# Performance work log

Measured on AMD Instinct MI355X. Metric: run time of the kernel, lower is better.

The kernel has to match this reference:

```python
import jax, jax.numpy as jnp
import numpy as np
import math

NUM_CLASSES = 80
IOU_LOSS_THRESH = 0.5
ANCHORS = [
    np.array([[12, 16], [19, 36], [40, 28]], dtype=np.float32),
    np.array([[36, 75], [76, 55], [72, 146]], dtype=np.float32),
    np.array([[142, 110], [192, 243], [459, 401]], dtype=np.float32),
]


def decode(conv, anchors, stride, num_class):
    B, S = conv.shape[0], conv.shape[1]
    A = anchors.shape[0]
    conv = conv.reshape(B, S, S, A, 5 + num_class)
    dxdy = conv[..., 0:2]
    dwdh = conv[..., 2:4]
    dconf = conv[..., 4:5]
    dprob = conv[..., 5:]
    r = jnp.arange(S, dtype=conv.dtype)
    # matches torch: offset[..., 0] varies along dim2, offset[..., 1] along dim1
    offset = jnp.stack([jnp.broadcast_to(r[None, :], (S, S)),
                        jnp.broadcast_to(r[:, None], (S, S))], axis=-1)
    offset = offset[None, :, :, None, :]  # (1,S,S,1,2)
    pred_xy = (jax.nn.sigmoid(dxdy) + offset) * stride
    pred_wh = jnp.exp(dwdh) * jnp.asarray(anchors)  # (A,2) broadcast
    return jnp.concatenate([pred_xy, pred_wh,
                            jax.nn.sigmoid(dconf), jax.nn.sigmoid(dprob)], axis=-1)


def _to_corners(b):
    return jnp.concatenate([b[..., :2] - b[..., 2:] * 0.5,
                            b[..., :2] + b[..., 2:] * 0.5], axis=-1)


def bbox_ciou(boxes1, boxes2):
    b1 = _to_corners(boxes1)
    b2 = _to_corners(boxes2)
    b1 = jnp.concatenate([jnp.minimum(b1[..., :2], b1[..., 2:]),
                          jnp.maximum(b1[..., :2], b1[..., 2:])], axis=-1)
    b2 = jnp.concatenate([jnp.minimum(b2[..., :2], b2[..., 2:]),
                          jnp.maximum(b2[..., :2], b2[..., 2:])], axis=-1)
    area1 = (b1[..., 2] - b1[..., 0]) * (b1[..., 3] - b1[..., 1])
    area2 = (b2[..., 2] - b2[..., 0]) * (b2[..., 3] - b2[..., 1])
    lu = jnp.maximum(b1[..., :2], b2[..., :2])
    rd = jnp.minimum(b1[..., 2:], b2[..., 2:])
    inter = jnp.maximum(rd - lu, 0.0)
    inter_area = inter[..., 0] * inter[..., 1]
    union = area1 + area2 - inter_area
    iou = inter_area / (union + 1e-9)
    enc_lu = jnp.minimum(b1[..., :2], b2[..., :2])
    enc_rd = jnp.maximum(b1[..., 2:], b2[..., 2:])
    enc_wh = enc_rd - enc_lu
    c2 = enc_wh[..., 0] ** 2 + enc_wh[..., 1] ** 2
    p2 = (boxes1[..., 0] - boxes2[..., 0]) ** 2 + (boxes1[..., 1] - boxes2[..., 1]) ** 2
    atan1 = jnp.arctan(boxes1[..., 2] / (boxes1[..., 3] + 1e-9))
    atan2 = jnp.arctan(boxes2[..., 2] / (boxes2[..., 3] + 1e-9))
    v = 4.0 * (atan1 - atan2) ** 2 / (math.pi ** 2)
    a = v / (1.0 - iou + v)
    return iou - p2 / c2 - a * v


def bbox_iou(boxes1, boxes2):
    area1 = boxes1[..., 2] * boxes1[..., 3]
    area2 = boxes2[..., 2] * boxes2[..., 3]
    b1 = _to_corners(boxes1)
    b2 = _to_corners(boxes2)
    lu = jnp.maximum(b1[..., :2], b2[..., :2])
    rd = jnp.minimum(b1[..., 2:], b2[..., 2:])
    inter = jnp.maximum(rd - lu, 0.0)
    inter_area = inter[..., 0] * inter[..., 1]
    union = area1 + area2 - inter_area
    return inter_area / union


def loss_layer(conv, pred, label, bboxes, stride, num_class, iou_loss_thresh):
    B, S = conv.shape[0], conv.shape[1]
    input_size = float(stride * S)
    pred_xywh = pred[..., 0:4]
    pred_conf = pred[..., 4:5]
    pred_prob = pred[..., 5:]
    label_xywh = label[..., 0:4]
    respond_bbox = label[..., 4:5]
    label_prob = label[..., 5:]

    ciou = bbox_ciou(pred_xywh, label_xywh)[..., None]  # (B,S,S,3,1)
    bbox_loss_scale = 2.0 - label_xywh[..., 2:3] * label_xywh[..., 3:4] / input_size ** 2
    ciou_loss = respond_bbox * bbox_loss_scale * (1.0 - ciou)

    prob_pos = label_prob * (-jnp.log(pred_prob + 1e-9))
    prob_neg = (1.0 - label_prob) * (-jnp.log(1.0 - pred_prob + 1e-9))
    prob_loss = respond_bbox * (prob_pos + prob_neg)

    iou = bbox_iou(pred_xywh[:, :, :, :, None, :],
                   bboxes[:, None, None, None, :, :])  # (B,S,S,3,70)
    max_iou = jnp.max(iou, axis=-1, keepdims=True)
    respond_bgd = (1.0 - respond_bbox) * (max_iou < iou_loss_thresh).astype(pred.dtype)
    pos_loss = respond_bbox * (-jnp.log(pred_conf + 1e-9))
    neg_loss = respond_bgd * (-jnp.log(1.0 - pred_conf + 1e-9))
    conf_loss = pos_loss + neg_loss

    ciou_loss = ciou_loss.sum(axis=(1, 2, 3, 4)).mean()
    conf_loss = conf_loss.sum(axis=(1, 2, 3, 4)).mean()
    prob_loss = prob_loss.sum(axis=(1, 2, 3, 4)).mean()
    return ciou_loss, conf_loss, prob_loss


def setup_inputs() -> dict:
    key = jax.random.key(0)
    ks = jax.random.split(key, 7)
    B, NC = 16, NUM_CLASSES
    C = 3 * (5 + NC)
    inp = {
        'conv_lbbox': jax.random.normal(ks[0], (B, 19, 19, C), jnp.float32),
        'conv_mbbox': jax.random.normal(ks[1], (B, 38, 38, C), jnp.float32),
        'conv_sbbox': jax.random.normal(ks[2], (B, 76, 76, C), jnp.float32),
        'label_sbbox': jax.random.uniform(ks[3], (B, 76, 76, 3, 5 + NC), jnp.float32),
        'label_mbbox': jax.random.uniform(ks[4], (B, 38, 38, 3, 5 + NC), jnp.float32),
        'label_lbbox': jax.random.uniform(ks[5], (B, 19, 19, 3, 5 + NC), jnp.float32),
        'true_bboxes': jax.random.uniform(ks[6], (B, 70, 4), jnp.float32, 1.0, 600.0),
    }
    return inp


def reference(conv_lbbox, conv_mbbox, conv_sbbox, label_sbbox, label_mbbox,
              label_lbbox, true_bboxes):
    nc, thr = NUM_CLASSES, IOU_LOSS_THRESH
    pred_s = decode(conv_sbbox, ANCHORS[0], 8, nc)
    pred_m = decode(conv_mbbox, ANCHORS[1], 16, nc)
    pred_l = decode(conv_lbbox, ANCHORS[2], 32, nc)
    s_ciou, s_conf, s_prob = loss_layer(conv_sbbox, pred_s, label_sbbox, true_bboxes, 8, nc, thr)
    m_ciou, m_conf, m_prob = loss_layer(conv_mbbox, pred_m, label_mbbox, true_bboxes, 16, nc, thr)
    l_ciou, l_conf, l_prob = loss_layer(conv_lbbox, pred_l, label_lbbox, true_bboxes, 32, nc, thr)
    ciou_loss = s_ciou + m_ciou + l_ciou
    conf_loss = s_conf + m_conf + l_conf
    prob_loss = s_prob + m_prob + l_prob
    all_loss = ciou_loss + conf_loss + prob_loss
    return (all_loss, ciou_loss, conf_loss, prob_loss)
```

## Files before the change

### kernel.cpp

```cpp
#include <hip/hip_runtime.h>
#include <math.h>

#define NCLS 80
#define CH 85

static constexpr int RS = 16 * 76 * 76 * 3;
static constexpr int RM = 16 * 38 * 38 * 3;
static constexpr int RL = 16 * 19 * 19 * 3;

static constexpr int RECB = 128;
static constexpr int BS_BLK = RS / RECB;
static constexpr int BM_BLK = (RM + RECB - 1) / RECB;
static constexpr int BL_BLK = (RL + RECB - 1) / RECB;
static constexpr int NBLK   = BS_BLK + BM_BLK + BL_BLK;

static constexpr int N4_FULL = RECB * CH / 4;
static constexpr int K_FULL  = N4_FULL / 256;
static constexpr int TAIL_T  = N4_FULL - K_FULL * 256;

__constant__ float c_anchors[18] = {
    12.f, 16.f, 19.f, 36.f, 40.f, 28.f,
    36.f, 75.f, 76.f, 55.f, 72.f, 146.f,
    142.f, 110.f, 192.f, 243.f, 459.f, 401.f
};

__device__ __forceinline__ float fast_rcp(float x) {
    return __builtin_amdgcn_rcpf(x);
}
__device__ __forceinline__ float sigm(float x) {
    return fast_rcp(1.f + __expf(-x));
}
__device__ __forceinline__ float softplusf(float x) {
    return fmaxf(x, 0.f) + __logf(1.f + __expf(-fabsf(x)));
}

__global__ __launch_bounds__(256, 6) void yolo_main(
    const float* __restrict__ conv_l, const float* __restrict__ conv_m,
    const float* __restrict__ conv_s, const float* __restrict__ lab_s,
    const float* __restrict__ lab_m, const float* __restrict__ lab_l,
    const float* __restrict__ tb, float* __restrict__ pb)
{
    int blk = blockIdx.x;

    const float* conv; const float* lab;
    int S; float stride; int ao; int blkLocal; int nrec_scale;
    if (blk < BS_BLK) {
        conv = conv_s; lab = lab_s; S = 76; stride = 8.f;  ao = 0;
        blkLocal = blk;                 nrec_scale = RS;
    } else if (blk < BS_BLK + BM_BLK) {
        conv = conv_m; lab = lab_m; S = 38; stride = 16.f; ao = 6;
        blkLocal = blk - BS_BLK;        nrec_scale = RM;
    } else {
        conv = conv_l; lab = lab_l; S = 19; stride = 32.f; ao = 12;
        blkLocal = blk - BS_BLK - BM_BLK; nrec_scale = RL;
    }

    int r0   = blkLocal * RECB;
    int nrec = min(RECB, nrec_scale - r0);
    int n4   = (nrec * CH) >> 2;

    const float* cbase = conv + (size_t)r0 * CH;
    const float* lbase = lab  + (size_t)r0 * CH;

    __shared__ float resp_s[RECB + 4];
    __shared__ float red[4][3];

    int t = threadIdx.x;

    float resp = 0.f;
    float c0 = 0.f, c1 = 0.f, c2v = 0.f, c3 = 0.f, c4 = 0.f;
    float l0 = 0.f, l1 = 0.f, l2 = 0.f, l3 = 0.f;
    if (t < nrec) {
        const float* cr = cbase + (size_t)t * CH;
        const float* lr = lbase + (size_t)t * CH;
        resp = lr[4];
        c0 = cr[0]; c1 = cr[1]; c2v = cr[2]; c3 = cr[3]; c4 = cr[4];
        l0 = lr[0]; l1 = lr[1]; l2 = lr[2]; l3 = lr[3];
    }
    if (t <= RECB) resp_s[t] = (t < nrec) ? resp : 0.f;
    __syncthreads();

    float prob_acc = 0.f;

    auto do4 = [&](int i4) {
        int e = i4 << 2;
        float4 cv = *reinterpret_cast<const float4*>(cbase + e);
        float4 lv = *reinterpret_cast<const float4*>(lbase + e);
        unsigned rA  = (unsigned)e / 85u;
        unsigned rem = (rA + 1u) * 85u - (unsigned)e;
        float respA = resp_s[rA];
        float respB = resp_s[rA + 1u];
        float r1v = (rem <= 1u) ? respB : respA;
        float r2v = (rem <= 2u) ? respB : respA;
        float r3v = (rem <= 3u) ? respB : respA;
        prob_acc = fmaf(respA, fmaf(-lv.x, cv.x, softplusf(cv.x)), prob_acc);
        prob_acc = fmaf(r1v,   fmaf(-lv.y, cv.y, softplusf(cv.y)), prob_acc);
        prob_acc = fmaf(r2v,   fmaf(-lv.z, cv.z, softplusf(cv.z)), prob_acc);
        prob_acc = fmaf(r3v,   fmaf(-lv.w, cv.w, softplusf(cv.w)), prob_acc);
    };

    if (n4 == N4_FULL) {
        #pragma unroll 5
        for (int k = 0; k < K_FULL; ++k) do4(t + 256 * k);
        if (t < TAIL_T) do4(t + 256 * K_FULL);
    } else {
        for (int i4 = t; i4 < n4; i4 += 256) do4(i4);
    }

    float ciou_acc = 0.f, conf_acc = 0.f;
    if (t < nrec) {
        float corr = fmaf(-l0,   c0,  softplusf(c0))
                   + fmaf(-l1,   c1,  softplusf(c1))
                   + fmaf(-l2,   c2v, softplusf(c2v))
                   + fmaf(-l3,   c3,  softplusf(c3))
                   + fmaf(-resp, c4,  softplusf(c4));
        prob_acc = fmaf(-resp, corr, prob_acc);

        unsigned rl = (unsigned)(r0 + t);
        unsigned a = rl % 3u; unsigned q = rl / 3u;
        unsigned j = q % (unsigned)S; q /= (unsigned)S;
        unsigned i = q % (unsigned)S; unsigned b = q / (unsigned)S;

        float lx = l0, ly = l1, lw = l2, lh = l3;

        float px = (sigm(c0) + (float)j) * stride;
        float py = (sigm(c1) + (float)i) * stride;
        float pw = __expf(c2v) * c_anchors[ao + 2 * a];
        float ph = __expf(c3)  * c_anchors[ao + 2 * a + 1];

        float hx = 0.5f * pw, hy = 0.5f * ph;
        float b1x1 = px - hx, b1y1 = py - hy, b1x2 = px + hx, b1y2 = py + hy;
        float hlx = 0.5f * lw, hly = 0.5f * lh;
        float b2x1 = lx - hlx, b2y1 = ly - hly, b2x2 = lx + hlx, b2y2 = ly + hly;

        float area1 = (b1x2 - b1x1) * (b1y2 - b1y1);
        float area2 = (b2x2 - b2x1) * (b2y2 - b2y1);
        float lux = fmaxf(b1x1, b2x1), luy = fmaxf(b1y1, b2y1);
        float rdx = fminf(b1x2, b2x2), rdy = fminf(b1y2, b2y2);
        float iw = fmaxf(rdx - lux, 0.f), ih = fmaxf(rdy - luy, 0.f);
        float inter = iw * ih;
        float uni = area1 + area2 - inter;
        float iou = inter / (uni + 1e-9f);

        float encw = fmaxf(b1x2, b2x2) - fminf(b1x1, b2x1);
        float ench = fmaxf(b1y2, b2y2) - fminf(b1y1, b2y1);
        float cc2 = encw * encw + ench * ench;
        float dx = px - lx, dy = py - ly;
        float p2 = dx * dx + dy * dy;
        float at1 = atanf(pw / (ph + 1e-9f));
        float at2 = atanf(lw / (lh + 1e-9f));
        float dat = at1 - at2;
        const float FOUR_OVER_PI2 = 0.40528473456935109f;
        float v = FOUR_OVER_PI2 * dat * dat;
        float al = v / (1.f - iou + v);
        float ciou = iou - p2 / cc2 - al * v;
        float bscale = 2.f - lw * lh * (1.f / (608.f * 608.f));
        ciou_acc = resp * bscale * (1.f - ciou);

        const float4* tb4 = reinterpret_cast<const float4*>(tb) + (size_t)b * 70;
        float parea = pw * ph;
        float maxiou = 0.f;
        #pragma unroll 5
        for (int n = 0; n < 70; n++) {
            float4 tbx = tb4[n];
            float tx = tbx.x, ty = tbx.y, tw = tbx.z, th = tbx.w;
            float tx1 = tx - 0.5f * tw, ty1 = ty - 0.5f * th;
            float tx2 = tx + 0.5f * tw, ty2 = ty + 0.5f * th;
            float ix1 = fmaxf(b1x1, tx1), iy1 = fmaxf(b1y1, ty1);
            float ix2 = fminf(b1x2, tx2), iy2 = fminf(b1y2, ty2);
            float iiw = fmaxf(ix2 - ix1, 0.f), iih = fmaxf(iy2 - iy1, 0.f);
            float ia = iiw * iih;
            float u = parea + tw * th - ia;
            maxiou = fmaxf(maxiou, ia * fast_rcp(u));
        }
        float rbgd = (1.f - resp) * (maxiou < 0.5f ? 1.f : 0.f);
        float spc = softplusf(c4);
        conf_acc = resp * (spc - c4) + rbgd * spc;
    }

    for (int off = 32; off > 0; off >>= 1) {
        ciou_acc += __shfl_down(ciou_acc, off);
        conf_acc += __shfl_down(conf_acc, off);
        prob_acc += __shfl_down(prob_acc, off);
    }
    int lane = threadIdx.x & 63, wv = threadIdx.x >> 6;
    if (lane == 0) { red[wv][0] = ciou_acc; red[wv][1] = conf_acc; red[wv][2] = prob_acc; }
    __syncthreads();
    if (threadIdx.x == 0) {
        pb[blk]            = red[0][0] + red[1][0] + red[2][0] + red[3][0];
        pb[NBLK + blk]     = red[0][1] + red[1][1] + red[2][1] + red[3][1];
        pb[2 * NBLK + blk] = red[0][2] + red[1][2] + red[2][2] + red[3][2];
    }
}

__global__ __launch_bounds__(256) void finalize_k(const float* __restrict__ pb,
                                                  float* __restrict__ out)
{
    double s0 = 0.0, s1 = 0.0, s2 = 0.0;
    for (int i = threadIdx.x; i < NBLK; i += 256) {
        s0 += (double)pb[i];
        s1 += (double)pb[NBLK + i];
        s2 += (double)pb[2 * NBLK + i];
    }
    for (int off = 32; off > 0; off >>= 1) {
        s0 += __shfl_down(s0, off);
        s1 += __shfl_down(s1, off);
        s2 += __shfl_down(s2, off);
    }
    __shared__ double rd[4][3];
    int lane = threadIdx.x & 63, wv = threadIdx.x >> 6;
    if (lane == 0) { rd[wv][0] = s0; rd[wv][1] = s1; rd[wv][2] = s2; }
    __syncthreads();
    if (threadIdx.x == 0) {
        float ci = (float)((rd[0][0] + rd[1][0] + rd[2][0] + rd[3][0]) / 16.0);
        float co = (float)((rd[0][1] + rd[1][1] + rd[2][1] + rd[3][1]) / 16.0);
        float pr = (float)((rd[0][2] + rd[1][2] + rd[2][2] + rd[3][2]) / 16.0);
        out[0] = ci + co + pr;
        out[1] = ci;
        out[2] = co;
        out[3] = pr;
    }
}

extern "C" void kernel_launch(void* const* d_in, const int* in_sizes, int n_in,
                              void* d_out, int out_size, void* d_ws, size_t ws_size,
                              hipStream_t stream) {
    const float* conv_l = (const float*)d_in[0];
    const float* conv_m = (const float*)d_in[1];
    const float* conv_s = (const float*)d_in[2];
    const float* lab_s  = (const float*)d_in[3];
    const float* lab_m  = (const float*)d_in[4];
    const float* lab_l  = (const float*)d_in[5];
    const float* tb     = (const float*)d_in[6];
    float* pb  = (float*)d_ws;
    float* out = (float*)d_out;

    yolo_main<<<NBLK, 256, 0, stream>>>(conv_l, conv_m, conv_s,
                                        lab_s, lab_m, lab_l, tb, pb);
    finalize_k<<<1, 256, 0, stream>>>(pb, out);
}
```

Baseline: 273.8 us.

## Software-pipeline prob loss loads and drop shared-memory resp staging barrier

After: 278.1 us. Within noise of the previous version (+1.6%).

```diff
diff --git a/kernel.cpp b/kernel.cpp
--- a/kernel.cpp
+++ b/kernel.cpp
@@ -1,7 +1,6 @@
 #include <hip/hip_runtime.h>
 #include <math.h>
 
-#define NCLS 80
 #define CH 85
 
 static constexpr int RS = 16 * 76 * 76 * 3;
@@ -15,7 +14,7 @@
 static constexpr int NBLK   = BS_BLK + BM_BLK + BL_BLK;
 
 static constexpr int N4_FULL = RECB * CH / 4;
-static constexpr int K_FULL  = N4_FULL / 256;
+static constexpr int K_FULL  = 10;
 static constexpr int TAIL_T  = N4_FULL - K_FULL * 256;
 
 __constant__ float c_anchors[18] = {
@@ -34,7 +33,54 @@
     return fmaxf(x, 0.f) + __logf(1.f + __expf(-fabsf(x)));
 }
 
-__global__ __launch_bounds__(256, 6) void yolo_main(
+
+template<int CNT>
+__device__ __forceinline__ void load_stage(const float* __restrict__ cbase,
+                                           const float* __restrict__ lbase,
+                                           int nrec, const int (&i4s)[CNT],
+                                           const bool (&act)[CNT],
+                                           float4 (&cv)[CNT], float4 (&lv)[CNT],
+                                           float (&ra)[CNT], float (&rb)[CNT])
+{
+    #pragma unroll
+    for (int u = 0; u < CNT; ++u) {
+        int e = i4s[u] << 2;
+        cv[u] = *reinterpret_cast<const float4*>(cbase + e);
+        lv[u] = *reinterpret_cast<const float4*>(lbase + e);
+        unsigned rA  = (unsigned)e / 85u;
+        unsigned rBi = rA + 1u;
+        unsigned rmx = (unsigned)(nrec - 1);
+        rBi = (rBi > rmx) ? rmx : rBi;
+        float a = lbase[rA * 85u + 4u];
+        float b = lbase[rBi * 85u + 4u];
+        ra[u] = act[u] ? a : 0.f;
+        rb[u] = act[u] ? b : 0.f;
+    }
+}
+
+template<int CNT>
+__device__ __forceinline__ void comp_stage(const int (&i4s)[CNT],
+                                           const float4 (&cv)[CNT], const float4 (&lv)[CNT],
+                                           const float (&ra)[CNT], const float (&rb)[CNT],
+                                           float& prob_acc)
+{
+    #pragma unroll
+    for (int u = 0; u < CNT; ++u) {
+        int e = i4s[u] << 2;
+        unsigned rA  = (unsigned)e / 85u;
+        unsigned rem = (rA + 1u) * 85u - (unsigned)e;
+        float respA = ra[u], respB = rb[u];
+        float r1 = (rem <= 1u) ? respB : respA;
+        float r2 = (rem <= 2u) ? respB : respA;
+        float r3 = (rem <= 3u) ? respB : respA;
+        prob_acc = fmaf(respA, fmaf(-lv[u].x, cv[u].x, softplusf(cv[u].x)), prob_acc);
+        prob_acc = fmaf(r1,    fmaf(-lv[u].y, cv[u].y, softplusf(cv[u].y)), prob_acc);
+        prob_acc = fmaf(r2,    fmaf(-lv[u].z, cv[u].z, softplusf(cv[u].z)), prob_acc);
+        prob_acc = fmaf(r3,    fmaf(-lv[u].w, cv[u].w, softplusf(cv[u].w)), prob_acc);
+    }
+}
+
+__global__ __launch_bounds__(256, 4) void yolo_main(
     const float* __restrict__ conv_l, const float* __restrict__ conv_m,
     const float* __restrict__ conv_s, const float* __restrict__ lab_s,
     const float* __restrict__ lab_m, const float* __restrict__ lab_l,
@@ -62,52 +108,64 @@
     const float* cbase = conv + (size_t)r0 * CH;
     const float* lbase = lab  + (size_t)r0 * CH;
 
-    __shared__ float resp_s[RECB + 4];
-    __shared__ float red[4][3];
-
     int t = threadIdx.x;
 
-    float resp = 0.f;
+    float prob_acc = 0.f, ciou_acc = 0.f, conf_acc = 0.f;
     float c0 = 0.f, c1 = 0.f, c2v = 0.f, c3 = 0.f, c4 = 0.f;
-    float l0 = 0.f, l1 = 0.f, l2 = 0.f, l3 = 0.f;
-    if (t < nrec) {
-        const float* cr = cbase + (size_t)t * CH;
-        const float* lr = lbase + (size_t)t * CH;
-        resp = lr[4];
-        c0 = cr[0]; c1 = cr[1]; c2v = cr[2]; c3 = cr[3]; c4 = cr[4];
-        l0 = lr[0]; l1 = lr[1]; l2 = lr[2]; l3 = lr[3];
-    }
-    if (t <= RECB) resp_s[t] = (t < nrec) ? resp : 0.f;
-    __syncthreads();
-
-    float prob_acc = 0.f;
-
-    auto do4 = [&](int i4) {
-        int e = i4 << 2;
-        float4 cv = *reinterpret_cast<const float4*>(cbase + e);
-        float4 lv = *reinterpret_cast<const float4*>(lbase + e);
-        unsigned rA  = (unsigned)e / 85u;
-        unsigned rem = (rA + 1u) * 85u - (unsigned)e;
-        float respA = resp_s[rA];
-        float respB = resp_s[rA + 1u];
-        float r1v = (rem <= 1u) ? respB : respA;
-        float r2v = (rem <= 2u) ? respB : respA;
-        float r3v = (rem <= 3u) ? respB : respA;
-        prob_acc = fmaf(respA, fmaf(-lv.x, cv.x, softplusf(cv.x)), prob_acc);
-        prob_acc = fmaf(r1v,   fmaf(-lv.y, cv.y, softplusf(cv.y)), prob_acc);
-        prob_acc = fmaf(r2v,   fmaf(-lv.z, cv.z, softplusf(cv.z)), prob_acc);
-        prob_acc = fmaf(r3v,   fmaf(-lv.w, cv.w, softplusf(cv.w)), prob_acc);
-    };
+    float l0 = 0.f, l1 = 0.f, l2 = 0.f, l3 = 0.f, resp = 0.f;
 
     if (n4 == N4_FULL) {
-        #pragma unroll 5
-        for (int k = 0; k < K_FULL; ++k) do4(t + 256 * k);
-        if (t < TAIL_T) do4(t + 256 * K_FULL);
+        int  iA[4] = { t,          t + 256,    t + 512,    t + 768  };
+        int  iB[4] = { t + 1024,   t + 1280,   t + 1536,   t + 1792 };
+        bool tl    = (t < TAIL_T);
+        int  iC[3] = { t + 2048,   t + 2304,   tl ? (t + 2560) : t };
+        bool a4[4] = { true, true, true, true };
+        bool aC[3] = { true, true, tl };
+
+        float4 cvA[4], lvA[4]; float raA[4], rbA[4];
+        float4 cvB[4], lvB[4]; float raB[4], rbB[4];
+        float4 cvC[3], lvC[3]; float raC[3], rbC[3];
+
+        load_stage<4>(cbase, lbase, nrec, iA, a4, cvA, lvA, raA, rbA);
+        load_stage<4>(cbase, lbase, nrec, iB, a4, cvB, lvB, raB, rbB);
+        comp_stage<4>(iA, cvA, lvA, raA, rbA, prob_acc);
+        load_stage<3>(cbase, lbase, nrec, iC, aC, cvC, lvC, raC, rbC);
+        comp_stage<4>(iB, cvB, lvB, raB, rbB, prob_acc);
+        if (t < RECB) {
+            const float* cr = cbase + t * CH;
+            const float* lr = lbase + t * CH;
+            c0 = cr[0]; c1 = cr[1]; c2v = cr[2]; c3 = cr[3]; c4 = cr[4];
+            l0 = lr[0]; l1 = lr[1]; l2  = lr[2]; l3 = lr[3]; resp = lr[4];
+        }
+        comp_stage<3>(iC, cvC, lvC, raC, rbC, prob_acc);
     } else {
-        for (int i4 = t; i4 < n4; i4 += 256) do4(i4);
-    }
-
-    float ciou_acc = 0.f, conf_acc = 0.f;
+        for (int i4 = t; i4 < n4; i4 += 256) {
+            int e = i4 << 2;
+            float4 cv = *reinterpret_cast<const float4*>(cbase + e);
+            float4 lv = *reinterpret_cast<const float4*>(lbase + e);
+            unsigned rA  = (unsigned)e / 85u;
+            unsigned rem = (rA + 1u) * 85u - (unsigned)e;
+            unsigned rBi = rA + 1u;
+            unsigned rmx = (unsigned)(nrec - 1);
+            rBi = (rBi > rmx) ? rmx : rBi;
+            float respA = lbase[rA * 85u + 4u];
+            float respB = lbase[rBi * 85u + 4u];
+            float r1 = (rem <= 1u) ? respB : respA;
+            float r2 = (rem <= 2u) ? respB : respA;
+            float r3 = (rem <= 3u) ? respB : respA;
+            prob_acc = fmaf(respA, fmaf(-lv.x, cv.x, softplusf(cv.x)), prob_acc);
+            prob_acc = fmaf(r1,    fmaf(-lv.y, cv.y, softplusf(cv.y)), prob_acc);
+            prob_acc = fmaf(r2,    fmaf(-lv.z, cv.z, softplusf(cv.z)), prob_acc);
+            prob_acc = fmaf(r3,    fmaf(-lv.w, cv.w, softplusf(cv.w)), prob_acc);
+        }
+        if (t < nrec) {
+            const float* cr = cbase + t * CH;
+            const float* lr = lbase + t * CH;
+            c0 = cr[0]; c1 = cr[1]; c2v = cr[2]; c3 = cr[3]; c4 = cr[4];
+            l0 = lr[0]; l1 = lr[1]; l2  = lr[2]; l3 = lr[3]; resp = lr[4];
+        }
+    }
+
     if (t < nrec) {
         float corr = fmaf(-l0,   c0,  softplusf(c0))
                    + fmaf(-l1,   c1,  softplusf(c1))
@@ -183,6 +241,7 @@
         conf_acc += __shfl_down(conf_acc, off);
         prob_acc += __shfl_down(prob_acc, off);
     }
+    __shared__ float red[4][3];
     int lane = threadIdx.x & 63, wv = threadIdx.x >> 6;
     if (lane == 0) { red[wv][0] = ciou_acc; red[wv][1] = conf_acc; red[wv][2] = prob_acc; }
     __syncthreads();
```

## Split kernel into grid-stride BCE blocks and per-record CIoU/conf blocks

Applied to the files above, without the earlier changes.

After: 273.9 us. No clear change (+0.0%).

```diff
diff --git a/kernel.cpp b/kernel.cpp
--- a/kernel.cpp
+++ b/kernel.cpp
@@ -1,22 +1,29 @@
 #include <hip/hip_runtime.h>
 #include <math.h>
 
-#define NCLS 80
 #define CH 85
 
 static constexpr int RS = 16 * 76 * 76 * 3;
 static constexpr int RM = 16 * 38 * 38 * 3;
 static constexpr int RL = 16 * 19 * 19 * 3;
-
-static constexpr int RECB = 128;
-static constexpr int BS_BLK = RS / RECB;
-static constexpr int BM_BLK = (RM + RECB - 1) / RECB;
-static constexpr int BL_BLK = (RL + RECB - 1) / RECB;
-static constexpr int NBLK   = BS_BLK + BM_BLK + BL_BLK;
-
-static constexpr int N4_FULL = RECB * CH / 4;
-static constexpr int K_FULL  = N4_FULL / 256;
-static constexpr int TAIL_T  = N4_FULL - K_FULL * 256;
+static constexpr int NREC = RS + RM + RL;
+
+static constexpr unsigned N4S  = (unsigned)RS * 85u / 4u;
+static constexpr unsigned N4M  = (unsigned)RM * 85u / 4u;
+static constexpr unsigned N4SM = N4S + N4M;
+static constexpr unsigned N4T  = N4SM + (unsigned)RL * 85u / 4u;
+
+static constexpr int NBLKA   = 2048;
+static constexpr int THRA    = NBLKA * 256;
+static constexpr int FULL_IT = (int)(N4T / (unsigned)THRA);
+static constexpr int REMA    = (int)(N4T - (unsigned)FULL_IT * (unsigned)THRA);
+
+static constexpr int NBLKB    = (NREC + 255) / 256;
+static constexpr int NBLK_TOT = NBLKA + NBLKB;
+
+static constexpr int PB_CIOU = NBLKA;
+static constexpr int PB_CONF = NBLKA + NBLKB;
+static constexpr int PB_PRB2 = NBLKA + 2 * NBLKB;
 
 __constant__ float c_anchors[18] = {
     12.f, 16.f, 19.f, 36.f, 40.f, 28.f,
@@ -34,148 +41,137 @@
     return fmaxf(x, 0.f) + __logf(1.f + __expf(-fabsf(x)));
 }
 
-__global__ __launch_bounds__(256, 6) void yolo_main(
+__device__ __forceinline__ void bce4(const float* __restrict__ cb,
+                                     const float* __restrict__ lb,
+                                     unsigned el, unsigned rmax, float& acc)
+{
+    float4 cv = *reinterpret_cast<const float4*>(cb + el);
+    float4 lv = *reinterpret_cast<const float4*>(lb + el);
+    unsigned rA  = el / 85u;
+    unsigned rem = (rA + 1u) * 85u - el;
+    unsigned rB  = rA + 1u; if (rB > rmax) rB = rmax;
+    float respA = lb[rA * 85u + 4u];
+    float respB = lb[rB * 85u + 4u];
+    float r1 = (rem <= 1u) ? respB : respA;
+    float r2 = (rem <= 2u) ? respB : respA;
+    float r3 = (rem <= 3u) ? respB : respA;
+    acc = fmaf(respA, fmaf(-lv.x, cv.x, softplusf(cv.x)), acc);
+    acc = fmaf(r1,    fmaf(-lv.y, cv.y, softplusf(cv.y)), acc);
+    acc = fmaf(r2,    fmaf(-lv.z, cv.z, softplusf(cv.z)), acc);
+    acc = fmaf(r3,    fmaf(-lv.w, cv.w, softplusf(cv.w)), acc);
+}
+
+__global__ __launch_bounds__(256) void yolo_main(
     const float* __restrict__ conv_l, const float* __restrict__ conv_m,
     const float* __restrict__ conv_s, const float* __restrict__ lab_s,
     const float* __restrict__ lab_m, const float* __restrict__ lab_l,
     const float* __restrict__ tb, float* __restrict__ pb)
 {
     int blk = blockIdx.x;
-
-    const float* conv; const float* lab;
-    int S; float stride; int ao; int blkLocal; int nrec_scale;
-    if (blk < BS_BLK) {
-        conv = conv_s; lab = lab_s; S = 76; stride = 8.f;  ao = 0;
-        blkLocal = blk;                 nrec_scale = RS;
-    } else if (blk < BS_BLK + BM_BLK) {
-        conv = conv_m; lab = lab_m; S = 38; stride = 16.f; ao = 6;
-        blkLocal = blk - BS_BLK;        nrec_scale = RM;
+    int t   = threadIdx.x;
+
+    float ciou_acc = 0.f, conf_acc = 0.f, prob_acc = 0.f;
+
+    if (blk < NBLKA) {
+        unsigned tid = (unsigned)(blk * 256 + t);
+
+        auto proc = [&](unsigned i4) {
+            const float* cb; const float* lb; unsigned el; unsigned rmax;
+            if (i4 < N4S)       { cb = conv_s; lb = lab_s; el = i4 * 4u;          rmax = (unsigned)RS - 1u; }
+            else if (i4 < N4SM) { cb = conv_m; lb = lab_m; el = (i4 - N4S) * 4u;  rmax = (unsigned)RM - 1u; }
+            else                { cb = conv_l; lb = lab_l; el = (i4 - N4SM) * 4u; rmax = (unsigned)RL - 1u; }
+            bce4(cb, lb, el, rmax, prob_acc);
+        };
+
+        #pragma unroll 4
+        for (int k = 0; k < FULL_IT; ++k)
+            proc(tid + (unsigned)k * (unsigned)THRA);
+        if (tid < (unsigned)REMA)
+            proc(tid + (unsigned)FULL_IT * (unsigned)THRA);
     } else {
-        conv = conv_l; lab = lab_l; S = 19; stride = 32.f; ao = 12;
-        blkLocal = blk - BS_BLK - BM_BLK; nrec_scale = RL;
-    }
-
-    int r0   = blkLocal * RECB;
-    int nrec = min(RECB, nrec_scale - r0);
-    int n4   = (nrec * CH) >> 2;
-
-    const float* cbase = conv + (size_t)r0 * CH;
-    const float* lbase = lab  + (size_t)r0 * CH;
-
-    __shared__ float resp_s[RECB + 4];
-    __shared__ float red[4][3];
-
-    int t = threadIdx.x;
-
-    float resp = 0.f;
-    float c0 = 0.f, c1 = 0.f, c2v = 0.f, c3 = 0.f, c4 = 0.f;
-    float l0 = 0.f, l1 = 0.f, l2 = 0.f, l3 = 0.f;
-    if (t < nrec) {
-        const float* cr = cbase + (size_t)t * CH;
-        const float* lr = lbase + (size_t)t * CH;
-        resp = lr[4];
-        c0 = cr[0]; c1 = cr[1]; c2v = cr[2]; c3 = cr[3]; c4 = cr[4];
-        l0 = lr[0]; l1 = lr[1]; l2 = lr[2]; l3 = lr[3];
-    }
-    if (t <= RECB) resp_s[t] = (t < nrec) ? resp : 0.f;
-    __syncthreads();
-
-    float prob_acc = 0.f;
-
-    auto do4 = [&](int i4) {
-        int e = i4 << 2;
-        float4 cv = *reinterpret_cast<const float4*>(cbase + e);
-        float4 lv = *reinterpret_cast<const float4*>(lbase + e);
-        unsigned rA  = (unsigned)e / 85u;
-        unsigned rem = (rA + 1u) * 85u - (unsigned)e;
-        float respA = resp_s[rA];
-        float respB = resp_s[rA + 1u];
-        float r1v = (rem <= 1u) ? respB : respA;
-        float r2v = (rem <= 2u) ? respB : respA;
-        float r3v = (rem <= 3u) ? respB : respA;
-        prob_acc = fmaf(respA, fmaf(-lv.x, cv.x, softplusf(cv.x)), prob_acc);
-        prob_acc = fmaf(r1v,   fmaf(-lv.y, cv.y, softplusf(cv.y)), prob_acc);
-        prob_acc = fmaf(r2v,   fmaf(-lv.z, cv.z, softplusf(cv.z)), prob_acc);
-        prob_acc = fmaf(r3v,   fmaf(-lv.w, cv.w, softplusf(cv.w)), prob_acc);
-    };
-
-    if (n4 == N4_FULL) {
-        #pragma unroll 5
-        for (int k = 0; k < K_FULL; ++k) do4(t + 256 * k);
-        if (t < TAIL_T) do4(t + 256 * K_FULL);
-    } else {
-        for (int i4 = t; i4 < n4; i4 += 256) do4(i4);
-    }
-
-    float ciou_acc = 0.f, conf_acc = 0.f;
-    if (t < nrec) {
-        float corr = fmaf(-l0,   c0,  softplusf(c0))
-                   + fmaf(-l1,   c1,  softplusf(c1))
-                   + fmaf(-l2,   c2v, softplusf(c2v))
-                   + fmaf(-l3,   c3,  softplusf(c3))
-                   + fmaf(-resp, c4,  softplusf(c4));
-        prob_acc = fmaf(-resp, corr, prob_acc);
-
-        unsigned rl = (unsigned)(r0 + t);
-        unsigned a = rl % 3u; unsigned q = rl / 3u;
-        unsigned j = q % (unsigned)S; q /= (unsigned)S;
-        unsigned i = q % (unsigned)S; unsigned b = q / (unsigned)S;
-
-        float lx = l0, ly = l1, lw = l2, lh = l3;
-
-        float px = (sigm(c0) + (float)j) * stride;
-        float py = (sigm(c1) + (float)i) * stride;
-        float pw = __expf(c2v) * c_anchors[ao + 2 * a];
-        float ph = __expf(c3)  * c_anchors[ao + 2 * a + 1];
-
-        float hx = 0.5f * pw, hy = 0.5f * ph;
-        float b1x1 = px - hx, b1y1 = py - hy, b1x2 = px + hx, b1y2 = py + hy;
-        float hlx = 0.5f * lw, hly = 0.5f * lh;
-        float b2x1 = lx - hlx, b2y1 = ly - hly, b2x2 = lx + hlx, b2y2 = ly + hly;
-
-        float area1 = (b1x2 - b1x1) * (b1y2 - b1y1);
-        float area2 = (b2x2 - b2x1) * (b2y2 - b2y1);
-        float lux = fmaxf(b1x1, b2x1), luy = fmaxf(b1y1, b2y1);
-        float rdx = fminf(b1x2, b2x2), rdy = fminf(b1y2, b2y2);
-        float iw = fmaxf(rdx - lux, 0.f), ih = fmaxf(rdy - luy, 0.f);
-        float inter = iw * ih;
-        float uni = area1 + area2 - inter;
-        float iou = inter / (uni + 1e-9f);
-
-        float encw = fmaxf(b1x2, b2x2) - fminf(b1x1, b2x1);
-        float ench = fmaxf(b1y2, b2y2) - fminf(b1y1, b2y1);
-        float cc2 = encw * encw + ench * ench;
-        float dx = px - lx, dy = py - ly;
-        float p2 = dx * dx + dy * dy;
-        float at1 = atanf(pw / (ph + 1e-9f));
-        float at2 = atanf(lw / (lh + 1e-9f));
-        float dat = at1 - at2;
-        const float FOUR_OVER_PI2 = 0.40528473456935109f;
-        float v = FOUR_OVER_PI2 * dat * dat;
-        float al = v / (1.f - iou + v);
-        float ciou = iou - p2 / cc2 - al * v;
-        float bscale = 2.f - lw * lh * (1.f / (608.f * 608.f));
-        ciou_acc = resp * bscale * (1.f - ciou);
-
-        const float4* tb4 = reinterpret_cast<const float4*>(tb) + (size_t)b * 70;
-        float parea = pw * ph;
-        float maxiou = 0.f;
-        #pragma unroll 5
-        for (int n = 0; n < 70; n++) {
-            float4 tbx = tb4[n];
-            float tx = tbx.x, ty = tbx.y, tw = tbx.z, th = tbx.w;
-            float tx1 = tx - 0.5f * tw, ty1 = ty - 0.5f * th;
-            float tx2 = tx + 0.5f * tw, ty2 = ty + 0.5f * th;
-            float ix1 = fmaxf(b1x1, tx1), iy1 = fmaxf(b1y1, ty1);
-            float ix2 = fminf(b1x2, tx2), iy2 = fminf(b1y2, ty2);
-            float iiw = fmaxf(ix2 - ix1, 0.f), iih = fmaxf(iy2 - iy1, 0.f);
-            float ia = iiw * iih;
-            float u = parea + tw * th - ia;
-            maxiou = fmaxf(maxiou, ia * fast_rcp(u));
+        int g = (blk - NBLKA) * 256 + t;
+        if (g < NREC) {
+            const float* conv; const float* lab;
+            int S; float stride; int ao; unsigned gl;
+            if (g < RS) {
+                conv = conv_s; lab = lab_s; S = 76; stride = 8.f;  ao = 0;  gl = (unsigned)g;
+            } else if (g < RS + RM) {
+                conv = conv_m; lab = lab_m; S = 38; stride = 16.f; ao = 6;  gl = (unsigned)(g - RS);
+            } else {
+                conv = conv_l; lab = lab_l; S = 19; stride = 32.f; ao = 12; gl = (unsigned)(g - RS - RM);
+            }
+            const float* cr = conv + (size_t)gl * CH;
+            const float* lr = lab  + (size_t)gl * CH;
+            float c0 = cr[0], c1 = cr[1], c2v = cr[2], c3 = cr[3], c4 = cr[4];
+            float l0 = lr[0], l1 = lr[1], l2  = lr[2], l3 = lr[3], resp = lr[4];
+
+            float corr = fmaf(-l0,   c0,  softplusf(c0))
+                       + fmaf(-l1,   c1,  softplusf(c1))
+                       + fmaf(-l2,   c2v, softplusf(c2v))
+                       + fmaf(-l3,   c3,  softplusf(c3))
+                       + fmaf(-resp, c4,  softplusf(c4));
+            prob_acc = -resp * corr;
+
+            unsigned a = gl % 3u; unsigned q = gl / 3u;
+            unsigned j = q % (unsigned)S; q /= (unsigned)S;
+            unsigned i = q % (unsigned)S; unsigned b = q / (unsigned)S;
+
+            float lx = l0, ly = l1, lw = l2, lh = l3;
+
+            float px = (sigm(c0) + (float)j) * stride;
+            float py = (sigm(c1) + (float)i) * stride;
+            float pw = __expf(c2v) * c_anchors[ao + 2 * a];
+            float ph = __expf(c3)  * c_anchors[ao + 2 * a + 1];
+
+            float hx = 0.5f * pw, hy = 0.5f * ph;
+            float b1x1 = px - hx, b1y1 = py - hy, b1x2 = px + hx, b1y2 = py + hy;
+            float hlx = 0.5f * lw, hly = 0.5f * lh;
+            float b2x1 = lx - hlx, b2y1 = ly - hly, b2x2 = lx + hlx, b2y2 = ly + hly;
+
+            float area1 = (b1x2 - b1x1) * (b1y2 - b1y1);
+            float area2 = (b2x2 - b2x1) * (b2y2 - b2y1);
+            float lux = fmaxf(b1x1, b2x1), luy = fmaxf(b1y1, b2y1);
+            float rdx = fminf(b1x2, b2x2), rdy = fminf(b1y2, b2y2);
+            float iw = fmaxf(rdx - lux, 0.f), ih = fmaxf(rdy - luy, 0.f);
+            float inter = iw * ih;
+            float uni = area1 + area2 - inter;
+            float iou = inter / (uni + 1e-9f);
+
+            float encw = fmaxf(b1x2, b2x2) - fminf(b1x1, b2x1);
+            float ench = fmaxf(b1y2, b2y2) - fminf(b1y1, b2y1);
+            float cc2 = encw * encw + ench * ench;
+            float dx = px - lx, dy = py - ly;
+            float p2 = dx * dx + dy * dy;
+            float at1 = atanf(pw / (ph + 1e-9f));
+            float at2 = atanf(lw / (lh + 1e-9f));
+            float dat = at1 - at2;
+            const float FOUR_OVER_PI2 = 0.40528473456935109f;
+            float v = FOUR_OVER_PI2 * dat * dat;
+            float al = v / (1.f - iou + v);
+            float ciou = iou - p2 / cc2 - al * v;
+            float bscale = 2.f - lw * lh * (1.f / (608.f * 608.f));
+            ciou_acc = resp * bscale * (1.f - ciou);
+
+            const float4* tb4 = reinterpret_cast<const float4*>(tb) + (size_t)b * 70;
+            float parea = pw * ph;
+            float maxiou = 0.f;
+            #pragma unroll 5
+            for (int n = 0; n < 70; n++) {
+                float4 tbx = tb4[n];
+                float tx = tbx.x, ty = tbx.y, tw = tbx.z, th = tbx.w;
+                float tx1 = tx - 0.5f * tw, ty1 = ty - 0.5f * th;
+                float tx2 = tx + 0.5f * tw, ty2 = ty + 0.5f * th;
+                float ix1 = fmaxf(b1x1, tx1), iy1 = fmaxf(b1y1, ty1);
+                float ix2 = fminf(b1x2, tx2), iy2 = fminf(b1y2, ty2);
+                float iiw = fmaxf(ix2 - ix1, 0.f), iih = fmaxf(iy2 - iy1, 0.f);
+                float ia = iiw * iih;
+                float u = parea + tw * th - ia;
+                maxiou = fmaxf(maxiou, ia * fast_rcp(u));
+            }
+            float rbgd = (1.f - resp) * (maxiou < 0.5f ? 1.f : 0.f);
+            float spc = softplusf(c4);
+            conf_acc = resp * (spc - c4) + rbgd * spc;
         }
-        float rbgd = (1.f - resp) * (maxiou < 0.5f ? 1.f : 0.f);
-        float spc = softplusf(c4);
-        conf_acc = resp * (spc - c4) + rbgd * spc;
     }
 
     for (int off = 32; off > 0; off >>= 1) {
@@ -183,13 +179,20 @@
         conf_acc += __shfl_down(conf_acc, off);
         prob_acc += __shfl_down(prob_acc, off);
     }
+    __shared__ float red[4][3];
     int lane = threadIdx.x & 63, wv = threadIdx.x >> 6;
     if (lane == 0) { red[wv][0] = ciou_acc; red[wv][1] = conf_acc; red[wv][2] = prob_acc; }
     __syncthreads();
     if (threadIdx.x == 0) {
-        pb[blk]            = red[0][0] + red[1][0] + red[2][0] + red[3][0];
-        pb[NBLK + blk]     = red[0][1] + red[1][1] + red[2][1] + red[3][1];
-        pb[2 * NBLK + blk] = red[0][2] + red[1][2] + red[2][2] + red[3][2];
+        float pr = red[0][2] + red[1][2] + red[2][2] + red[3][2];
+        if (blk < NBLKA) {
+            pb[blk] = pr;
+        } else {
+            int gb = blk - NBLKA;
+            pb[PB_CIOU + gb] = red[0][0] + red[1][0] + red[2][0] + red[3][0];
+            pb[PB_CONF + gb] = red[0][1] + red[1][1] + red[2][1] + red[3][1];
+            pb[PB_PRB2 + gb] = pr;
+        }
     }
 }
 
@@ -197,10 +200,12 @@
                                                   float* __restrict__ out)
 {
     double s0 = 0.0, s1 = 0.0, s2 = 0.0;
-    for (int i = threadIdx.x; i < NBLK; i += 256) {
-        s0 += (double)pb[i];
-        s1 += (double)pb[NBLK + i];
-        s2 += (double)pb[2 * NBLK + i];
+    for (int i = threadIdx.x; i < NBLKA; i += 256)
+        s2 += (double)pb[i];
+    for (int i = threadIdx.x; i < NBLKB; i += 256) {
+        s0 += (double)pb[PB_CIOU + i];
+        s1 += (double)pb[PB_CONF + i];
+        s2 += (double)pb[PB_PRB2 + i];
     }
     for (int off = 32; off > 0; off >>= 1) {
         s0 += __shfl_down(s0, off);
@@ -235,7 +240,7 @@
     float* pb  = (float*)d_ws;
     float* out = (float*)d_out;
 
-    yolo_main<<<NBLK, 256, 0, stream>>>(conv_l, conv_m, conv_s,
-                                        lab_s, lab_m, lab_l, tb, pb);
+    yolo_main<<<NBLK_TOT, 256, 0, stream>>>(conv_l, conv_m, conv_s,
+                                            lab_s, lab_m, lab_l, tb, pb);
     finalize_k<<<1, 256, 0, stream>>>(pb, out);
 }
```
